# Optimization experiments

Hardware: AMD Instinct MI355X
Metric: run time of the kernel (lower is better)

The kernel has to match this reference:

```python
import jax, jax.numpy as jnp
import numpy as np


def _maxpool2(x):
    # 2x2 max pool, stride 2. x: (B, C, H, W)
    B, C, H, W = x.shape
    return x.reshape(B, C, H // 2, 2, W // 2, 2).max(axis=(3, 5))


def setup_inputs() -> dict:
    key = jax.random.key(0)
    ks = jax.random.split(key, 5)
    B, C, H, W = 16, 64, 64, 64
    x = jax.random.normal(ks[0], (B, C, H, W), dtype=jnp.float32)
    Wq = jax.random.normal(ks[1], (C // 8, C), dtype=jnp.float32) * 0.05
    Wk = jax.random.normal(ks[2], (C // 8, C), dtype=jnp.float32) * 0.05
    Wv = jax.random.normal(ks[3], (C // 2, C), dtype=jnp.float32) * 0.05
    Wo = jax.random.normal(ks[4], (C, C // 2), dtype=jnp.float32) * 0.05
    gamma = jnp.float32(0.5)
    return {"x": x, "Wq": Wq, "Wk": Wk, "Wv": Wv, "Wo": Wo, "gamma": gamma}


def reference(x, Wq, Wk, Wv, Wo, gamma):
    B, C, H, W = x.shape
    # 1x1 convs (bias=False) == channel-mixing einsums
    q = jnp.einsum('oc,bchw->bohw', Wq, x)                 # (B, C/8, H, W)
    k = _maxpool2(jnp.einsum('oc,bchw->bohw', Wk, x))      # (B, C/8, H/2, W/2)
    v = _maxpool2(jnp.einsum('oc,bchw->bohw', Wv, x))      # (B, C/2, H/2, W/2)
    q = q.reshape(B, C // 8, H * W)
    k = k.reshape(B, C // 8, H * W // 4)
    v = v.reshape(B, C // 2, H * W // 4)
    # scores: (B, HW, HW/4), softmax over pooled KV axis
    w = jax.nn.softmax(jnp.einsum('bcn,bcm->bnm', q, k), axis=-1)
    o = jnp.einsum('bcm,bnm->bcn', v, w).reshape(B, C // 2, H, W)
    o = jnp.einsum('oc,bchw->bohw', Wo, o)                 # (B, C, H, W)
    return gamma * o + x
```

## Files before the change

kernel.cpp:

```cpp
#include <hip/hip_runtime.h>
#include <hip/hip_bf16.h>

typedef __attribute__((ext_vector_type(8))) short short8;
typedef __attribute__((ext_vector_type(4))) float f32x4;

#define LOG2E 1.4426950408889634f

__device__ __forceinline__ unsigned short f2bf(float f) {
    unsigned int u = __float_as_uint(f);
    u = (u + 0x7FFFu + ((u >> 16) & 1u)) >> 16;
    return (unsigned short)u;
}
__device__ __forceinline__ unsigned int pack2(float a, float b) {
    return (unsigned int)f2bf(a) | ((unsigned int)f2bf(b) << 16);
}
__device__ __forceinline__ float bf2f(unsigned short s) {
    return __uint_as_float((unsigned int)s << 16);
}
__device__ __forceinline__ float fast_exp2(float x) {
#if __has_builtin(__builtin_amdgcn_exp2f)
    return __builtin_amdgcn_exp2f(x);
#else
    return __expf(x * 0.6931471805599453f);
#endif
}
__device__ __forceinline__ unsigned int cvt_pk_bf16(float lo, float hi) {
    unsigned int r;
    asm("v_cvt_pk_bf16_f32 %0, %1, %2" : "=v"(r) : "v"(lo), "v"(hi));
    return r;
}

__global__ __launch_bounds__(512, 4) void proj_pool_kernel(
    const float* __restrict__ x, const float* __restrict__ Wq,
    const float* __restrict__ Wk, const float* __restrict__ Wv,
    unsigned short* __restrict__ q_ws, unsigned short* __restrict__ k_ws,
    unsigned short* __restrict__ v_t)
{
    __shared__ __align__(16) char smem[45056];
    float* xs   = (float*)smem;
    float* wt   = (float*)(smem + 32768);
    short* kvsm = (short*)smem;
    short* vtr  = (short*)(smem + 16384);

    const int b = blockIdx.x >> 5, s = blockIdx.x & 31;
    const int t = threadIdx.x;

    for (int idx = t; idx < 3072; idx += 512) {
        const int c = idx / 48, j = idx - c * 48;
        float w;
        if (j < 8)       w = Wq[j * 64 + c] * (LOG2E * 0.25f);
        else if (j < 16) w = Wk[(j - 8) * 64 + c];
        else             w = Wv[(j - 16) * 64 + c];
        wt[idx] = w;
    }
    {
        const float* xsrc = x + (size_t)b * 262144 + s * 128;
#pragma unroll
        for (int r = 0; r < 4; ++r) {
            const int chunk = r * 512 + t;
            const int c = chunk >> 5, nn = (chunk & 31) * 4;
            *(float4*)&xs[c * 128 + nn] = *(const float4*)&xsrc[(size_t)c * 4096 + nn];
        }
    }
    __syncthreads();

    const int tn = t & 127, og = t >> 7;
    float acc[12];
#pragma unroll
    for (int j = 0; j < 12; ++j) acc[j] = 0.f;
#pragma unroll 8
    for (int c = 0; c < 64; ++c) {
        const float xv = xs[c * 128 + tn];
        const float4* wr = (const float4*)&wt[c * 48 + og * 12];
#pragma unroll
        for (int j4 = 0; j4 < 3; ++j4) {
            const float4 w = wr[j4];
            acc[j4 * 4 + 0] = fmaf(xv, w.x, acc[j4 * 4 + 0]);
            acc[j4 * 4 + 1] = fmaf(xv, w.y, acc[j4 * 4 + 1]);
            acc[j4 * 4 + 2] = fmaf(xv, w.z, acc[j4 * 4 + 2]);
            acc[j4 * 4 + 3] = fmaf(xv, w.w, acc[j4 * 4 + 3]);
        }
    }
    if (og == 0) {
        uint4 qo;
        qo.x = pack2(acc[0], acc[1]); qo.y = pack2(acc[2], acc[3]);
        qo.z = pack2(acc[4], acc[5]); qo.w = pack2(acc[6], acc[7]);
        *(uint4*)(q_ws + (size_t)(b * 4096 + s * 128 + tn) * 8) = qo;
    }
    __syncthreads();

    {
        const int kvbase = (og == 0) ? 0 : og * 12 - 8;
        const int abase  = (og == 0) ? 8 : 0;
        const int cnt2   = (og == 0) ? 2 : 6;
        unsigned int* dst = (unsigned int*)&kvsm[tn * 44 + kvbase];
#pragma unroll
        for (int p = 0; p < 6; ++p)
            if (p < cnt2) dst[p] = pack2(acc[abase + 2 * p], acc[abase + 2 * p + 1]);
    }
    __syncthreads();

    if (t < 320) {
        const int mw = t & 31, chp = t >> 5;
        union U4 { uint2 v; unsigned short sh[4]; };
        U4 a0, a1, a2, a3;
        a0.v = *(const uint2*)&kvsm[(2 * mw)      * 44 + chp * 4];
        a1.v = *(const uint2*)&kvsm[(2 * mw + 1)  * 44 + chp * 4];
        a2.v = *(const uint2*)&kvsm[(2 * mw + 64) * 44 + chp * 4];
        a3.v = *(const uint2*)&kvsm[(2 * mw + 65) * 44 + chp * 4];
        unsigned short r[4];
#pragma unroll
        for (int j = 0; j < 4; ++j) {
            const float m01 = fmaxf(bf2f(a0.sh[j]), bf2f(a1.sh[j]));
            const float m23 = fmaxf(bf2f(a2.sh[j]), bf2f(a3.sh[j]));
            r[j] = (unsigned short)(__float_as_uint(fmaxf(m01, m23)) >> 16);
        }
        const int m = s * 32 + mw;
        if (chp < 2) {
            uint2 ko;
            ko.x = (unsigned int)r[0] | ((unsigned int)r[1] << 16);
            ko.y = (unsigned int)r[2] | ((unsigned int)r[3] << 16);
            *(uint2*)(k_ws + (size_t)(b * 1024 + m) * 8 + chp * 4) = ko;
        } else {
            const int cv = chp * 4 - 8;
#pragma unroll
            for (int j = 0; j < 4; ++j) vtr[(cv + j) * 36 + mw] = (short)r[j];
        }
    }
    __syncthreads();

    if (t < 256) {
        const int cv = t >> 3, seg = t & 7;
        const uint2 vv = *(const uint2*)&vtr[cv * 36 + seg * 4];
        *(uint2*)(v_t + ((size_t)(b * 32 + cv) << 10) + s * 32 + seg * 4) = vv;
    }
}

__global__ __launch_bounds__(512, 4) void attn_out_kernel(
    const unsigned short* __restrict__ q_ws, const unsigned short* __restrict__ k_ws,
    const unsigned short* __restrict__ v_t, const float* __restrict__ Wo,
    const float* __restrict__ x, const float* __restrict__ gamma_p,
    float* __restrict__ out)
{
    __shared__ __align__(16) char smem[81920];
    short* Klds = (short*)smem;
    char*  Vb   = smem + 16384;

    const int b = blockIdx.x >> 5, n0 = (blockIdx.x & 31) * 128;
    const int t = threadIdx.x;
    const int wid = t >> 6, lane = t & 63;
    const int l16 = lane & 15, g4 = lane >> 4;

    union { uint4 u4; short8 s8; } qf;
    qf.u4 = *(const uint4*)(q_ws + (size_t)(b * 4096 + n0 + wid * 16 + l16) * 8);

#pragma unroll
    for (int p = 0; p < 2; ++p) {
        const int mg = p * 512 + t;
        const uint4 kr = *(const uint4*)(k_ws + (size_t)(b * 1024 + mg) * 8);
        const int row = (mg & ~31) | (((mg >> 2) & 1) << 4) | (((mg >> 3) & 3) << 2) | (mg & 3);
        *(uint4*)&Klds[row * 8] = kr;
    }
    {
        const char* vsrc = (const char*)(v_t + ((size_t)b << 15));
#pragma unroll
        for (int k8 = 0; k8 < 8; ++k8) {
            const int B = (k8 * 512 + t) * 16;
            const uint4 vv = *(const uint4*)(vsrc + B);
            const int cv = B >> 11, off = B & 2047;
            *(uint4*)(Vb + cv * 2048 + (off ^ ((cv & 7) << 4))) = vv;
        }
    }

    f32x4 acc0 = {0.f, 0.f, 0.f, 0.f};
    f32x4 acc1 = {0.f, 0.f, 0.f, 0.f};
    float l_run = 0.f;

    __syncthreads();

    for (int ch = 0; ch < 4; ++ch) {
#pragma unroll
        for (int grp = 0; grp < 2; ++grp) {
            float sg[32];
#pragma unroll
            for (int u = 0; u < 4; ++u) {
                const int rb = ch * 256 + grp * 128 + u * 32;
                const short8 A0 = *(const short8*)&Klds[(rb + l16) * 8];
                const short8 A1 = *(const short8*)&Klds[(rb + 16 + l16) * 8];
                const f32x4 z = {0.f, 0.f, 0.f, 0.f};
                const f32x4 sA = __builtin_amdgcn_mfma_f32_16x16x32_bf16(A0, qf.s8, z, 0, 0, 0);
                const f32x4 sB = __builtin_amdgcn_mfma_f32_16x16x32_bf16(A1, qf.s8, z, 0, 0, 0);
#pragma unroll
                for (int i = 0; i < 4; ++i) { sg[u * 8 + i] = sA[i]; sg[u * 8 + 4 + i] = sB[i]; }
            }
            float ps0 = 0.f, ps1 = 0.f, ps2 = 0.f, ps3 = 0.f;
#pragma unroll
            for (int i = 0; i < 32; i += 4) {
                sg[i + 0] = fast_exp2(sg[i + 0]); ps0 += sg[i + 0];
                sg[i + 1] = fast_exp2(sg[i + 1]); ps1 += sg[i + 1];
                sg[i + 2] = fast_exp2(sg[i + 2]); ps2 += sg[i + 2];
                sg[i + 3] = fast_exp2(sg[i + 3]); ps3 += sg[i + 3];
            }
            l_run += (ps0 + ps1) + (ps2 + ps3);
#pragma unroll
            for (int u = 0; u < 4; ++u) {
                union { unsigned int w[4]; short8 s8; } pb;
                pb.w[0] = cvt_pk_bf16(sg[u * 8 + 0], sg[u * 8 + 1]);
                pb.w[1] = cvt_pk_bf16(sg[u * 8 + 2], sg[u * 8 + 3]);
                pb.w[2] = cvt_pk_bf16(sg[u * 8 + 4], sg[u * 8 + 5]);
                pb.w[3] = cvt_pk_bf16(sg[u * 8 + 6], sg[u * 8 + 7]);
                const int moff = (ch * 256 + grp * 128 + u * 32 + g4 * 8) * 2;
                const int sw0 = (l16 & 7) << 4;
                const short8 va0 = *(const short8*)(Vb + l16 * 2048 + (moff ^ sw0));
                const short8 va1 = *(const short8*)(Vb + (l16 + 16) * 2048 + (moff ^ sw0));
                acc0 = __builtin_amdgcn_mfma_f32_16x16x32_bf16(va0, pb.s8, acc0, 0, 0, 0);
                acc1 = __builtin_amdgcn_mfma_f32_16x16x32_bf16(va1, pb.s8, acc1, 0, 0, 0);
            }
        }
    }

    {
        float l2 = l_run + __shfl_xor(l_run, 16);
        l2 = l2 + __shfl_xor(l2, 32);
        const float inv = 1.0f / l2;
        acc0 *= inv; acc1 *= inv;
    }

    __syncthreads();
    f32x4* o4 = (f32x4*)smem;
    float* wo_lds = (float*)Vb;
    {
        const int nloc = wid * 16 + l16;
        o4[nloc * 8 + ((g4    ) ^ (nloc & 7))] = acc0;
        o4[nloc * 8 + ((g4 + 4) ^ (nloc & 7))] = acc1;
    }
    for (int idx = t; idx < 2048; idx += 512) wo_lds[idx] = Wo[idx];
    __syncthreads();

    const float gv = gamma_p[0];
    const int n2 = t & 127;
    const int cg = t >> 7;
    float oc[32];
#pragma unroll
    for (int q8 = 0; q8 < 8; ++q8) {
        const f32x4 v = o4[n2 * 8 + (q8 ^ (n2 & 7))];
        const int cvb = (q8 >> 2) * 16 + (q8 & 3) * 4;
        oc[cvb + 0] = v[0]; oc[cvb + 1] = v[1]; oc[cvb + 2] = v[2]; oc[cvb + 3] = v[3];
    }
#pragma unroll
    for (int j = 0; j < 16; ++j) {
        const int c = cg * 16 + j;
        const f32x4* w4 = (const f32x4*)&wo_lds[c * 32];
        float a = 0.f;
#pragma unroll
        for (int q8 = 0; q8 < 8; ++q8) {
            const f32x4 w = w4[q8];
            a += oc[q8 * 4 + 0] * w[0] + oc[q8 * 4 + 1] * w[1]
               + oc[q8 * 4 + 2] * w[2] + oc[q8 * 4 + 3] * w[3];
        }
        const size_t oidx = ((size_t)(b * 64 + c) << 12) + n0 + n2;
        out[oidx] = fmaf(gv, a, x[oidx]);
    }
}

extern "C" void kernel_launch(void* const* d_in, const int* in_sizes, int n_in,
                              void* d_out, int out_size, void* d_ws, size_t ws_size,
                              hipStream_t stream) {
    const float* x     = (const float*)d_in[0];
    const float* Wq    = (const float*)d_in[1];
    const float* Wk    = (const float*)d_in[2];
    const float* Wv    = (const float*)d_in[3];
    const float* Wo    = (const float*)d_in[4];
    const float* gamma = (const float*)d_in[5];
    float* out = (float*)d_out;

    char* ws = (char*)d_ws;
    unsigned short* q_ws = (unsigned short*)ws;
    unsigned short* k_ws = (unsigned short*)(ws + (1 << 20));
    unsigned short* v_t  = (unsigned short*)(ws + (1 << 20) + (256 << 10));

    proj_pool_kernel<<<dim3(512), dim3(512), 0, stream>>>(x, Wq, Wk, Wv, q_ws, k_ws, v_t);
    attn_out_kernel<<<dim3(512), dim3(512), 0, stream>>>(q_ws, k_ws, v_t, Wo, x, gamma, out);
}
```

Measured before the change: 41.56 us.

## Use MFMA for projections and process two query tiles per attention wave

The projection kernel now converts x to bf16 in a swizzled transposed LDS layout and computes the Q/K/V 1x1 convs with bf16 MFMA, replacing the fp32 scalar FMA loop, and uses 256-thread blocks. The attention kernel gives each wave two 16-row query tiles so every K and V fragment loaded from LDS is reused across both, and it halves the grid to 256 blocks of 256 queries. This cuts LDS traffic and the staging cost of K/V per query, at the cost of fewer blocks to fill the GPU's compute units and bf16 rounding of x and the weights in the projection.

```diff
diff --git a/kernel.cpp b/kernel.cpp
--- a/kernel.cpp
+++ b/kernel.cpp
@@ -6,14 +6,6 @@
 
 #define LOG2E 1.4426950408889634f
 
-__device__ __forceinline__ unsigned short f2bf(float f) {
-    unsigned int u = __float_as_uint(f);
-    u = (u + 0x7FFFu + ((u >> 16) & 1u)) >> 16;
-    return (unsigned short)u;
-}
-__device__ __forceinline__ unsigned int pack2(float a, float b) {
-    return (unsigned int)f2bf(a) | ((unsigned int)f2bf(b) << 16);
-}
 __device__ __forceinline__ float bf2f(unsigned short s) {
     return __uint_as_float((unsigned int)s << 16);
 }
@@ -30,109 +22,121 @@
     return r;
 }
 
-__global__ __launch_bounds__(512, 4) void proj_pool_kernel(
+__global__ __launch_bounds__(256, 2) void proj_pool_kernel(
     const float* __restrict__ x, const float* __restrict__ Wq,
     const float* __restrict__ Wk, const float* __restrict__ Wv,
     unsigned short* __restrict__ q_ws, unsigned short* __restrict__ k_ws,
     unsigned short* __restrict__ v_t)
 {
-    __shared__ __align__(16) char smem[45056];
-    float* xs   = (float*)smem;
-    float* wt   = (float*)(smem + 32768);
-    short* kvsm = (short*)smem;
-    short* vtr  = (short*)(smem + 16384);
+    __shared__ __align__(16) char smem[28672];
+    char* xT = smem;
+    unsigned int* kv = (unsigned int*)(smem + 16384);
 
     const int b = blockIdx.x >> 5, s = blockIdx.x & 31;
+    const int n0 = s * 128;
     const int t = threadIdx.x;
-
-    for (int idx = t; idx < 3072; idx += 512) {
-        const int c = idx / 48, j = idx - c * 48;
-        float w;
-        if (j < 8)       w = Wq[j * 64 + c] * (LOG2E * 0.25f);
-        else if (j < 16) w = Wk[(j - 8) * 64 + c];
-        else             w = Wv[(j - 16) * 64 + c];
-        wt[idx] = w;
-    }
-    {
-        const float* xsrc = x + (size_t)b * 262144 + s * 128;
-#pragma unroll
-        for (int r = 0; r < 4; ++r) {
-            const int chunk = r * 512 + t;
-            const int c = chunk >> 5, nn = (chunk & 31) * 4;
-            *(float4*)&xs[c * 128 + nn] = *(const float4*)&xsrc[(size_t)c * 4096 + nn];
-        }
-    }
-    __syncthreads();
-
-    const int tn = t & 127, og = t >> 7;
-    float acc[12];
-#pragma unroll
-    for (int j = 0; j < 12; ++j) acc[j] = 0.f;
-#pragma unroll 8
-    for (int c = 0; c < 64; ++c) {
-        const float xv = xs[c * 128 + tn];
-        const float4* wr = (const float4*)&wt[c * 48 + og * 12];
-#pragma unroll
-        for (int j4 = 0; j4 < 3; ++j4) {
-            const float4 w = wr[j4];
-            acc[j4 * 4 + 0] = fmaf(xv, w.x, acc[j4 * 4 + 0]);
-            acc[j4 * 4 + 1] = fmaf(xv, w.y, acc[j4 * 4 + 1]);
-            acc[j4 * 4 + 2] = fmaf(xv, w.z, acc[j4 * 4 + 2]);
-            acc[j4 * 4 + 3] = fmaf(xv, w.w, acc[j4 * 4 + 3]);
-        }
-    }
-    if (og == 0) {
-        uint4 qo;
-        qo.x = pack2(acc[0], acc[1]); qo.y = pack2(acc[2], acc[3]);
-        qo.z = pack2(acc[4], acc[5]); qo.w = pack2(acc[6], acc[7]);
-        *(uint4*)(q_ws + (size_t)(b * 4096 + s * 128 + tn) * 8) = qo;
-    }
-    __syncthreads();
-
-    {
-        const int kvbase = (og == 0) ? 0 : og * 12 - 8;
-        const int abase  = (og == 0) ? 8 : 0;
-        const int cnt2   = (og == 0) ? 2 : 6;
-        unsigned int* dst = (unsigned int*)&kvsm[tn * 44 + kvbase];
-#pragma unroll
-        for (int p = 0; p < 6; ++p)
-            if (p < cnt2) dst[p] = pack2(acc[abase + 2 * p], acc[abase + 2 * p + 1]);
-    }
-    __syncthreads();
-
-    if (t < 320) {
-        const int mw = t & 31, chp = t >> 5;
-        union U4 { uint2 v; unsigned short sh[4]; };
-        U4 a0, a1, a2, a3;
-        a0.v = *(const uint2*)&kvsm[(2 * mw)      * 44 + chp * 4];
-        a1.v = *(const uint2*)&kvsm[(2 * mw + 1)  * 44 + chp * 4];
-        a2.v = *(const uint2*)&kvsm[(2 * mw + 64) * 44 + chp * 4];
-        a3.v = *(const uint2*)&kvsm[(2 * mw + 65) * 44 + chp * 4];
-        unsigned short r[4];
-#pragma unroll
-        for (int j = 0; j < 4; ++j) {
-            const float m01 = fmaxf(bf2f(a0.sh[j]), bf2f(a1.sh[j]));
-            const float m23 = fmaxf(bf2f(a2.sh[j]), bf2f(a3.sh[j]));
-            r[j] = (unsigned short)(__float_as_uint(fmaxf(m01, m23)) >> 16);
-        }
-        const int m = s * 32 + mw;
-        if (chp < 2) {
-            uint2 ko;
-            ko.x = (unsigned int)r[0] | ((unsigned int)r[1] << 16);
-            ko.y = (unsigned int)r[2] | ((unsigned int)r[3] << 16);
-            *(uint2*)(k_ws + (size_t)(b * 1024 + m) * 8 + chp * 4) = ko;
+    const int w = t >> 6, lane = t & 63;
+    const int l16 = lane & 15, g4 = lane >> 4;
+
+    short8 wf[3][2];
+#pragma unroll
+    for (int tile = 0; tile < 3; ++tile) {
+        const float* wrow;
+        float scale = 1.0f;
+        if (tile == 0) {
+            if (l16 < 8) { wrow = Wq + l16 * 64; scale = LOG2E * 0.25f; }
+            else         { wrow = Wk + (l16 - 8) * 64; }
+        } else if (tile == 1) wrow = Wv + l16 * 64;
+        else                  wrow = Wv + (16 + l16) * 64;
+#pragma unroll
+        for (int ks = 0; ks < 2; ++ks) {
+            const float4 wa = *(const float4*)(wrow + ks * 32 + g4 * 8);
+            const float4 wb = *(const float4*)(wrow + ks * 32 + g4 * 8 + 4);
+            union { unsigned int u[4]; short8 s8; } uu;
+            uu.u[0] = cvt_pk_bf16(wa.x * scale, wa.y * scale);
+            uu.u[1] = cvt_pk_bf16(wa.z * scale, wa.w * scale);
+            uu.u[2] = cvt_pk_bf16(wb.x * scale, wb.y * scale);
+            uu.u[3] = cvt_pk_bf16(wb.z * scale, wb.w * scale);
+            wf[tile][ks] = uu.s8;
+        }
+    }
+
+    {
+        const int nloc = (w & 1) * 64 + lane;
+        const int cbase = (w >> 1) * 32;
+        const float* xp = x + (size_t)b * 262144 + (size_t)cbase * 4096 + n0 + nloc;
+        unsigned int pk[16];
+#pragma unroll
+        for (int j = 0; j < 16; ++j) {
+            const float e0 = xp[(size_t)(2 * j) * 4096];
+            const float e1 = xp[(size_t)(2 * j + 1) * 4096];
+            pk[j] = cvt_pk_bf16(e0, e1);
+        }
+        char* row = xT + nloc * 128;
+        const int sw = (nloc & 7) << 4;
+#pragma unroll
+        for (int h = 0; h < 4; ++h) {
+            const uint4 u = make_uint4(pk[h*4+0], pk[h*4+1], pk[h*4+2], pk[h*4+3]);
+            *(uint4*)(row + ((((cbase >> 3) + h) * 16) ^ sw)) = u;
+        }
+    }
+    __syncthreads();
+
+#pragma unroll
+    for (int p = 0; p < 2; ++p) {
+        const int tile = w * 2 + p;
+        const int nl = tile * 16 + l16;
+        f32x4 C0 = {0,0,0,0}, C1 = {0,0,0,0}, C2 = {0,0,0,0};
+#pragma unroll
+        for (int ks = 0; ks < 2; ++ks) {
+            const short8 xb = *(const short8*)(xT + nl * 128 + ((((ks*4+g4)*16)) ^ ((l16&7)<<4)));
+            C0 = __builtin_amdgcn_mfma_f32_16x16x32_bf16(wf[0][ks], xb, C0, 0, 0, 0);
+            C1 = __builtin_amdgcn_mfma_f32_16x16x32_bf16(wf[1][ks], xb, C1, 0, 0, 0);
+            C2 = __builtin_amdgcn_mfma_f32_16x16x32_bf16(wf[2][ks], xb, C2, 0, 0, 0);
+        }
+        const unsigned int c0lo = cvt_pk_bf16(C0[0], C0[1]);
+        const unsigned int c0hi = cvt_pk_bf16(C0[2], C0[3]);
+        if (g4 < 2) {
+            *(uint2*)(q_ws + (size_t)(b * 4096 + n0 + nl) * 8 + g4 * 4) = make_uint2(c0lo, c0hi);
         } else {
-            const int cv = chp * 4 - 8;
-#pragma unroll
-            for (int j = 0; j < 4; ++j) vtr[(cv + j) * 36 + mw] = (short)r[j];
-        }
-    }
-    __syncthreads();
-
-    if (t < 256) {
-        const int cv = t >> 3, seg = t & 7;
-        const uint2 vv = *(const uint2*)&vtr[cv * 36 + seg * 4];
-        *(uint2*)(v_t + ((size_t)(b * 32 + cv) << 10) + s * 32 + seg * 4) = vv;
+            *(uint2*)&kv[nl * 24 + (g4 - 2) * 2] = make_uint2(c0lo, c0hi);
+        }
+        *(uint2*)&kv[nl * 24 + 4 + g4 * 2] =
+            make_uint2(cvt_pk_bf16(C1[0], C1[1]), cvt_pk_bf16(C1[2], C1[3]));
+        *(uint2*)&kv[nl * 24 + 12 + g4 * 2] =
+            make_uint2(cvt_pk_bf16(C2[0], C2[1]), cvt_pk_bf16(C2[2], C2[3]));
+    }
+    __syncthreads();
+
+    if (t < 128) {
+        const int m = t >> 2, cg = t & 3;
+        const int r0 = m * 2, r2 = m * 2 + 64;
+        const int mg = s * 32 + m;
+        unsigned int res[5];
+#pragma unroll
+        for (int i = 0; i < 5; ++i) {
+            const unsigned int a  = kv[(r0    ) * 24 + cg * 5 + i];
+            const unsigned int b1 = kv[(r0 + 1) * 24 + cg * 5 + i];
+            const unsigned int c  = kv[(r2    ) * 24 + cg * 5 + i];
+            const unsigned int d  = kv[(r2 + 1) * 24 + cg * 5 + i];
+            const float lo = fmaxf(fmaxf(bf2f(a & 0xffff), bf2f(b1 & 0xffff)),
+                                   fmaxf(bf2f(c & 0xffff), bf2f(d & 0xffff)));
+            const float hi = fmaxf(fmaxf(bf2f(a >> 16), bf2f(b1 >> 16)),
+                                   fmaxf(bf2f(c >> 16), bf2f(d >> 16)));
+            res[i] = (__float_as_uint(lo) >> 16) | (__float_as_uint(hi) & 0xffff0000u);
+        }
+        if (cg == 0) {
+            *(uint4*)(k_ws + (size_t)(b * 1024 + mg) * 8) = make_uint4(res[0], res[1], res[2], res[3]);
+            v_t[((size_t)(b * 32 + 0) << 10) + mg] = (unsigned short)(res[4] & 0xffff);
+            v_t[((size_t)(b * 32 + 1) << 10) + mg] = (unsigned short)(res[4] >> 16);
+        } else {
+            const int cvb = cg * 10 - 8;
+#pragma unroll
+            for (int i = 0; i < 5; ++i) {
+                v_t[((size_t)(b * 32 + cvb + 2*i    ) << 10) + mg] = (unsigned short)(res[i] & 0xffff);
+                v_t[((size_t)(b * 32 + cvb + 2*i + 1) << 10) + mg] = (unsigned short)(res[i] >> 16);
+            }
+        }
     }
 }
 
@@ -146,13 +150,14 @@
     short* Klds = (short*)smem;
     char*  Vb   = smem + 16384;
 
-    const int b = blockIdx.x >> 5, n0 = (blockIdx.x & 31) * 128;
+    const int b = blockIdx.x >> 4, n0 = (blockIdx.x & 15) * 256;
     const int t = threadIdx.x;
     const int wid = t >> 6, lane = t & 63;
     const int l16 = lane & 15, g4 = lane >> 4;
 
-    union { uint4 u4; short8 s8; } qf;
-    qf.u4 = *(const uint4*)(q_ws + (size_t)(b * 4096 + n0 + wid * 16 + l16) * 8);
+    union { uint4 u4; short8 s8; } qfA, qfB;
+    qfA.u4 = *(const uint4*)(q_ws + (size_t)(b * 4096 + n0 + wid * 32 + l16) * 8);
+    qfB.u4 = *(const uint4*)(q_ws + (size_t)(b * 4096 + n0 + wid * 32 + 16 + l16) * 8);
 
 #pragma unroll
     for (int p = 0; p < 2; ++p) {
@@ -165,81 +170,79 @@
         const char* vsrc = (const char*)(v_t + ((size_t)b << 15));
 #pragma unroll
         for (int k8 = 0; k8 < 8; ++k8) {
-            const int B = (k8 * 512 + t) * 16;
-            const uint4 vv = *(const uint4*)(vsrc + B);
-            const int cv = B >> 11, off = B & 2047;
+            const int byt = (k8 * 512 + t) * 16;
+            const uint4 vv = *(const uint4*)(vsrc + byt);
+            const int cv = byt >> 11, off = byt & 2047;
             *(uint4*)(Vb + cv * 2048 + (off ^ ((cv & 7) << 4))) = vv;
         }
     }
 
-    f32x4 acc0 = {0.f, 0.f, 0.f, 0.f};
-    f32x4 acc1 = {0.f, 0.f, 0.f, 0.f};
-    float l_run = 0.f;
-
-    __syncthreads();
-
-    for (int ch = 0; ch < 4; ++ch) {
-#pragma unroll
-        for (int grp = 0; grp < 2; ++grp) {
-            float sg[32];
-#pragma unroll
-            for (int u = 0; u < 4; ++u) {
-                const int rb = ch * 256 + grp * 128 + u * 32;
-                const short8 A0 = *(const short8*)&Klds[(rb + l16) * 8];
-                const short8 A1 = *(const short8*)&Klds[(rb + 16 + l16) * 8];
-                const f32x4 z = {0.f, 0.f, 0.f, 0.f};
-                const f32x4 sA = __builtin_amdgcn_mfma_f32_16x16x32_bf16(A0, qf.s8, z, 0, 0, 0);
-                const f32x4 sB = __builtin_amdgcn_mfma_f32_16x16x32_bf16(A1, qf.s8, z, 0, 0, 0);
-#pragma unroll
-                for (int i = 0; i < 4; ++i) { sg[u * 8 + i] = sA[i]; sg[u * 8 + 4 + i] = sB[i]; }
-            }
-            float ps0 = 0.f, ps1 = 0.f, ps2 = 0.f, ps3 = 0.f;
-#pragma unroll
-            for (int i = 0; i < 32; i += 4) {
-                sg[i + 0] = fast_exp2(sg[i + 0]); ps0 += sg[i + 0];
-                sg[i + 1] = fast_exp2(sg[i + 1]); ps1 += sg[i + 1];
-                sg[i + 2] = fast_exp2(sg[i + 2]); ps2 += sg[i + 2];
-                sg[i + 3] = fast_exp2(sg[i + 3]); ps3 += sg[i + 3];
-            }
-            l_run += (ps0 + ps1) + (ps2 + ps3);
-#pragma unroll
-            for (int u = 0; u < 4; ++u) {
-                union { unsigned int w[4]; short8 s8; } pb;
-                pb.w[0] = cvt_pk_bf16(sg[u * 8 + 0], sg[u * 8 + 1]);
-                pb.w[1] = cvt_pk_bf16(sg[u * 8 + 2], sg[u * 8 + 3]);
-                pb.w[2] = cvt_pk_bf16(sg[u * 8 + 4], sg[u * 8 + 5]);
-                pb.w[3] = cvt_pk_bf16(sg[u * 8 + 6], sg[u * 8 + 7]);
-                const int moff = (ch * 256 + grp * 128 + u * 32 + g4 * 8) * 2;
-                const int sw0 = (l16 & 7) << 4;
-                const short8 va0 = *(const short8*)(Vb + l16 * 2048 + (moff ^ sw0));
-                const short8 va1 = *(const short8*)(Vb + (l16 + 16) * 2048 + (moff ^ sw0));
-                acc0 = __builtin_amdgcn_mfma_f32_16x16x32_bf16(va0, pb.s8, acc0, 0, 0, 0);
-                acc1 = __builtin_amdgcn_mfma_f32_16x16x32_bf16(va1, pb.s8, acc1, 0, 0, 0);
-            }
-        }
-    }
-
-    {
-        float l2 = l_run + __shfl_xor(l_run, 16);
-        l2 = l2 + __shfl_xor(l2, 32);
+    f32x4 a0A = {0,0,0,0}, a1A = {0,0,0,0}, a0B = {0,0,0,0}, a1B = {0,0,0,0};
+    float lA = 0.f, lB = 0.f;
+    __syncthreads();
+
+    const int rsw = (l16 & 7) << 4;
+    for (int sl = 0; sl < 32; ++sl) {
+        const int rb = sl * 32;
+        const short8 A0 = *(const short8*)&Klds[(rb + l16) * 8];
+        const short8 A1 = *(const short8*)&Klds[(rb + 16 + l16) * 8];
+        const f32x4 z = {0,0,0,0};
+        const f32x4 sA0 = __builtin_amdgcn_mfma_f32_16x16x32_bf16(A0, qfA.s8, z, 0, 0, 0);
+        const f32x4 sA1 = __builtin_amdgcn_mfma_f32_16x16x32_bf16(A1, qfA.s8, z, 0, 0, 0);
+        const f32x4 sB0 = __builtin_amdgcn_mfma_f32_16x16x32_bf16(A0, qfB.s8, z, 0, 0, 0);
+        const f32x4 sB1 = __builtin_amdgcn_mfma_f32_16x16x32_bf16(A1, qfB.s8, z, 0, 0, 0);
+
+        float eA[8], eB[8];
+        float psA = 0.f, psB = 0.f;
+#pragma unroll
+        for (int i = 0; i < 4; ++i) {
+            eA[i]     = fast_exp2(sA0[i]); psA += eA[i];
+            eA[4 + i] = fast_exp2(sA1[i]); psA += eA[4 + i];
+            eB[i]     = fast_exp2(sB0[i]); psB += eB[i];
+            eB[4 + i] = fast_exp2(sB1[i]); psB += eB[4 + i];
+        }
+        lA += psA; lB += psB;
+
+        union { unsigned int u[4]; short8 s8; } pbA, pbB;
+        pbA.u[0] = cvt_pk_bf16(eA[0], eA[1]); pbA.u[1] = cvt_pk_bf16(eA[2], eA[3]);
+        pbA.u[2] = cvt_pk_bf16(eA[4], eA[5]); pbA.u[3] = cvt_pk_bf16(eA[6], eA[7]);
+        pbB.u[0] = cvt_pk_bf16(eB[0], eB[1]); pbB.u[1] = cvt_pk_bf16(eB[2], eB[3]);
+        pbB.u[2] = cvt_pk_bf16(eB[4], eB[5]); pbB.u[3] = cvt_pk_bf16(eB[6], eB[7]);
+
+        const int moff = rb * 2 + g4 * 16;
+        const short8 va0 = *(const short8*)(Vb + l16 * 2048 + (moff ^ rsw));
+        const short8 va1 = *(const short8*)(Vb + (l16 + 16) * 2048 + (moff ^ rsw));
+        a0A = __builtin_amdgcn_mfma_f32_16x16x32_bf16(va0, pbA.s8, a0A, 0, 0, 0);
+        a1A = __builtin_amdgcn_mfma_f32_16x16x32_bf16(va1, pbA.s8, a1A, 0, 0, 0);
+        a0B = __builtin_amdgcn_mfma_f32_16x16x32_bf16(va0, pbB.s8, a0B, 0, 0, 0);
+        a1B = __builtin_amdgcn_mfma_f32_16x16x32_bf16(va1, pbB.s8, a1B, 0, 0, 0);
+    }
+
+    {
+        float l2 = lA + __shfl_xor(lA, 16); l2 += __shfl_xor(l2, 32);
         const float inv = 1.0f / l2;
-        acc0 *= inv; acc1 *= inv;
-    }
-
-    __syncthreads();
-    f32x4* o4 = (f32x4*)smem;
-    float* wo_lds = (float*)Vb;
-    {
-        const int nloc = wid * 16 + l16;
-        o4[nloc * 8 + ((g4    ) ^ (nloc & 7))] = acc0;
-        o4[nloc * 8 + ((g4 + 4) ^ (nloc & 7))] = acc1;
+        a0A *= inv; a1A *= inv;
+        float l3 = lB + __shfl_xor(lB, 16); l3 += __shfl_xor(l3, 32);
+        const float inv2 = 1.0f / l3;
+        a0B *= inv2; a1B *= inv2;
+    }
+
+    __syncthreads();
+    f32x4* o4 = (f32x4*)Vb;
+    float* wo_lds = (float*)Klds;
+    {
+        const int nlA = wid * 32 + l16, nlB = nlA + 16;
+        o4[nlA * 8 + ((g4    ) ^ (nlA & 7))] = a0A;
+        o4[nlA * 8 + ((g4 + 4) ^ (nlA & 7))] = a1A;
+        o4[nlB * 8 + ((g4    ) ^ (nlB & 7))] = a0B;
+        o4[nlB * 8 + ((g4 + 4) ^ (nlB & 7))] = a1B;
     }
     for (int idx = t; idx < 2048; idx += 512) wo_lds[idx] = Wo[idx];
     __syncthreads();
 
     const float gv = gamma_p[0];
-    const int n2 = t & 127;
-    const int cg = t >> 7;
+    const int n2 = t & 255;
+    const int cg = t >> 8;
     float oc[32];
 #pragma unroll
     for (int q8 = 0; q8 < 8; ++q8) {
@@ -248,15 +251,15 @@
         oc[cvb + 0] = v[0]; oc[cvb + 1] = v[1]; oc[cvb + 2] = v[2]; oc[cvb + 3] = v[3];
     }
 #pragma unroll
-    for (int j = 0; j < 16; ++j) {
-        const int c = cg * 16 + j;
+    for (int j = 0; j < 32; ++j) {
+        const int c = cg * 32 + j;
         const f32x4* w4 = (const f32x4*)&wo_lds[c * 32];
         float a = 0.f;
 #pragma unroll
         for (int q8 = 0; q8 < 8; ++q8) {
-            const f32x4 w = w4[q8];
-            a += oc[q8 * 4 + 0] * w[0] + oc[q8 * 4 + 1] * w[1]
-               + oc[q8 * 4 + 2] * w[2] + oc[q8 * 4 + 3] * w[3];
+            const f32x4 wv = w4[q8];
+            a += oc[q8 * 4 + 0] * wv[0] + oc[q8 * 4 + 1] * wv[1]
+               + oc[q8 * 4 + 2] * wv[2] + oc[q8 * 4 + 3] * wv[3];
         }
         const size_t oidx = ((size_t)(b * 64 + c) << 12) + n0 + n2;
         out[oidx] = fmaf(gv, a, x[oidx]);
@@ -279,6 +282,6 @@
     unsigned short* k_ws = (unsigned short*)(ws + (1 << 20));
     unsigned short* v_t  = (unsigned short*)(ws + (1 << 20) + (256 << 10));
 
-    proj_pool_kernel<<<dim3(512), dim3(512), 0, stream>>>(x, Wq, Wk, Wv, q_ws, k_ws, v_t);
-    attn_out_kernel<<<dim3(512), dim3(512), 0, stream>>>(q_ws, k_ws, v_t, Wo, x, gamma, out);
-}
+    proj_pool_kernel<<<dim3(512), dim3(256), 0, stream>>>(x, Wq, Wk, Wv, q_ws, k_ws, v_t);
+    attn_out_kernel<<<dim3(256), dim3(512), 0, stream>>>(q_ws, k_ws, v_t, Wo, x, gamma, out);
+}
```

Result: faster. 35.37 us (-14.9%).
